# Kernel optimization log

Hardware: AMD Instinct MI355X
Metric: run time of the kernel (lower is better)

Reference implementation:

```python
import jax, jax.numpy as jnp
from jax import lax
import numpy as np

BITS = 16
KSHAPE = (3, 5, 5)
STRIDE = (1, 1, 1)
PAD = (0, 0, 0)
IMG = (2048, 2048)


def setup_inputs() -> dict:
    key = jax.random.key(0)
    k1, k2 = jax.random.split(key)
    x = jax.random.randint(k1, IMG, 0, 2 ** BITS, dtype=jnp.int32)
    weight = jax.random.uniform(k2, KSHAPE, dtype=jnp.float32)
    bias = jnp.zeros((1,), dtype=jnp.float32)
    return {"x": x, "weight": weight, "bias": bias}


def reference(x, weight, bias):
    pad_d, pad_h, pad_w = PAD
    # spatial zero-padding of the integer image
    xp = jnp.pad(x, ((pad_h, pad_h), (pad_w, pad_w)))
    # bit-plane volume: V[z] = bit z of each pixel. (x << pad_d >> s) % 2
    # equals bit (s - pad_d) of x, and is 0 for s < pad_d, i.e. depth
    # zero-padding by pad_d on both sides of the BITS bit-planes.
    z = jnp.arange(BITS, dtype=jnp.int32)
    V = ((xp[None, :, :] >> z[:, None, None]) & 1).astype(jnp.float32)
    V = jnp.pad(V, ((pad_d, pad_d), (0, 0), (0, 0)))  # [D, Hp, Wp]
    # 3D cross-correlation (lax conv does not flip the kernel)
    Y = lax.conv_general_dilated(
        V[None, None],               # [1,1,D,Hp,Wp]
        weight[None, None],          # [1,1,d,h,w]
        window_strides=STRIDE,
        padding="VALID",
        dimension_numbers=("NCDHW", "OIDHW", "NCDHW"),
    )[0, 0]                          # [D_out, H_out, W_out]
    return Y + bias
```

## Files before the change

kernel.cpp:

```cpp
#include <hip/hip_runtime.h>

#define IMG_W 2048
#define IMG_H 2048
#define OUT_W 2044
#define OUT_H 2044
#define OUT_HW (2044 * 2044)

#define TI 16
#define TJ 64
#define LR (TI + 4)
#define LC (TJ + 4)
#define LSTR 69

typedef int v4i __attribute__((ext_vector_type(4)));

__global__ void quant_frag(const float* __restrict__ w, v4i* __restrict__ wfrag) {
    const int l = threadIdx.x;
    const int m = l & 15, g = l >> 4;
    #pragma unroll
    for (int t = 0; t < 7; ++t) {
        const int p = 4 * t + g;
        unsigned lo[4] = {0, 0, 0, 0}, hi[4] = {0, 0, 0, 0};
        if (p < 25 && m < 14) {
            const int kh = p / 5, kw = p % 5;
            #pragma unroll
            for (int kd = 0; kd < 3; ++kd) {
                const int e = m + kd;
                const unsigned w8 = (unsigned)(int)rintf(w[(kd * 5 + kh) * 5 + kw] * 255.0f);
                lo[e >> 2] |= (w8 & 15u) << (8 * (e & 3));
                hi[e >> 2] |= (w8 >> 4)  << (8 * (e & 3));
            }
        }
        v4i vlo, vhi;
        vlo.x = (int)lo[0]; vlo.y = (int)lo[1]; vlo.z = (int)lo[2]; vlo.w = (int)lo[3];
        vhi.x = (int)hi[0]; vhi.y = (int)hi[1]; vhi.z = (int)hi[2]; vhi.w = (int)hi[3];
        wfrag[t * 64 + l]       = vlo;
        wfrag[448 + t * 64 + l] = vhi;
    }
}

__global__ __launch_bounds__(256, 3) void conv_mfma(
        const int* __restrict__ x, const v4i* __restrict__ wfrag,
        const float* __restrict__ bias, float* __restrict__ out) {
    __shared__ v4i vt[LR * LSTR];
    const int tid  = threadIdx.x;
    const int lane = tid & 63;
    const int wv   = tid >> 6;
    const int m16  = lane & 15;
    const int g4   = lane >> 4;
    const int I0 = blockIdx.y * TI;
    const int J0 = blockIdx.x * TJ;

    v4i alo[7], ahi[7];
    #pragma unroll
    for (int t = 0; t < 7; ++t) {
        alo[t] = wfrag[t * 64 + lane];
        ahi[t] = wfrag[448 + t * 64 + lane];
    }
    const float b0 = bias[0];

    #pragma unroll
    for (int rr = 0; rr < 5; ++rr) {
        const int r  = wv + rr * 4;
        const int gr = min(I0 + r, IMG_H - 1);
        const long rowoff = (long)gr * IMG_W;
        #pragma unroll
        for (int cc = 0; cc < 2; ++cc) {
            const int col = lane + cc * 64;
            if (col < LC) {
                const int gc = min(J0 + col, IMG_W - 1);
                const unsigned v = (unsigned)x[rowoff + gc];
                v4i e;
                e.x = (int)(__umul24( v         & 0xFu, 0x00204081u) & 0x01010101u);
                e.y = (int)(__umul24((v >> 4)   & 0xFu, 0x00204081u) & 0x01010101u);
                e.z = (int)(__umul24((v >> 8)   & 0xFu, 0x00204081u) & 0x01010101u);
                e.w = (int)(__umul24((v >> 12)  & 0xFu, 0x00204081u) & 0x01010101u);
                vt[r * LSTR + col] = e;
            }
        }
    }
    __syncthreads();

    int koff[7];
    #pragma unroll
    for (int t = 0; t < 7; ++t) {
        const int p  = 4 * t + g4;
        const int kh = (p < 25) ? (p / 5) : 0;
        const int kw = (p < 25) ? (p - kh * 5) : 0;
        koff[t] = kh * LSTR + kw;
    }

    const float scale = 1.0f / 255.0f;

    #pragma unroll 1
    for (int ig = 0; ig < 4; ++ig) {
        const int il = wv * 4 + ig;
        const int i  = I0 + il;
        #pragma unroll 1
        for (int jg = 0; jg < 4; ++jg) {
            const int jb    = jg * 16 + m16;
            const int gbase = il * LSTR + jb;
            v4i bf[7];
            #pragma unroll
            for (int t = 0; t < 7; ++t) bf[t] = vt[gbase + koff[t]];

            v4i al0 = {0,0,0,0}, al1 = {0,0,0,0}, ah0 = {0,0,0,0}, ah1 = {0,0,0,0};
            #pragma unroll
            for (int t = 0; t < 6; t += 2) {
                al0 = __builtin_amdgcn_mfma_i32_16x16x64_i8(alo[t],     bf[t],     al0, 0, 0, 0);
                ah0 = __builtin_amdgcn_mfma_i32_16x16x64_i8(ahi[t],     bf[t],     ah0, 0, 0, 0);
                al1 = __builtin_amdgcn_mfma_i32_16x16x64_i8(alo[t + 1], bf[t + 1], al1, 0, 0, 0);
                ah1 = __builtin_amdgcn_mfma_i32_16x16x64_i8(ahi[t + 1], bf[t + 1], ah1, 0, 0, 0);
            }
            al0 = __builtin_amdgcn_mfma_i32_16x16x64_i8(alo[6], bf[6], al0, 0, 0, 0);
            ah0 = __builtin_amdgcn_mfma_i32_16x16x64_i8(ahi[6], bf[6], ah0, 0, 0, 0);

            const int j = J0 + jb;
            if (i < OUT_H && j < OUT_W) {
                #pragma unroll
                for (int r = 0; r < 4; ++r) {
                    const int d = g4 * 4 + r;
                    if (d < 14) {
                        const int acc = (ah0[r] + ah1[r]) * 16 + (al0[r] + al1[r]);
                        out[(size_t)d * OUT_HW + (size_t)i * OUT_W + j] =
                            fmaf((float)acc, scale, b0);
                    }
                }
            }
        }
    }
}

extern "C" void kernel_launch(void* const* d_in, const int* in_sizes, int n_in,
                              void* d_out, int out_size, void* d_ws, size_t ws_size,
                              hipStream_t stream) {
    const int* x      = (const int*)d_in[0];
    const float* w    = (const float*)d_in[1];
    const float* bias = (const float*)d_in[2];
    float* out        = (float*)d_out;
    v4i* wfrag        = (v4i*)d_ws;

    quant_frag<<<1, 64, 0, stream>>>(w, wfrag);
    conv_mfma<<<dim3((OUT_W + TJ - 1) / TJ, (OUT_H + TI - 1) / TI), 256, 0, stream>>>(
        x, wfrag, bias, out);
}
```

Before: 301.5 us.

## Stage conv outputs through LDS transpose for fully coalesced row stores

Each wave now writes its MFMA results for a row into a padded per-wave LDS buffer, then reads them back transposed. Each lane can then store one output column across the 14 depth planes, so every store instruction covers 64 contiguous floats instead of four scattered 16-float segments. This targets global write efficiency on the very large output tensor. It adds LDS traffic and LDS footprint, lowers the launch-bounds occupancy hint from 3 to 2, and fully unrolls the jg loop. The 16-byte vector writes at a row stride of 17 floats may be misaligned for ds_write_b128.

```diff
diff --git a/kernel.cpp b/kernel.cpp
--- a/kernel.cpp
+++ b/kernel.cpp
@@ -11,8 +11,10 @@
 #define LR (TI + 4)
 #define LC (TJ + 4)
 #define LSTR 69
+#define TRP 17
 
 typedef int v4i __attribute__((ext_vector_type(4)));
+typedef float v4f __attribute__((ext_vector_type(4)));
 
 __global__ void quant_frag(const float* __restrict__ w, v4i* __restrict__ wfrag) {
     const int l = threadIdx.x;
@@ -39,10 +41,11 @@
     }
 }
 
-__global__ __launch_bounds__(256, 3) void conv_mfma(
+__global__ __launch_bounds__(256, 2) void conv_mfma(
         const int* __restrict__ x, const v4i* __restrict__ wfrag,
         const float* __restrict__ bias, float* __restrict__ out) {
     __shared__ v4i vt[LR * LSTR];
+    __shared__ float trp[4 * 64 * TRP];
     const int tid  = threadIdx.x;
     const int lane = tid & 63;
     const int wv   = tid >> 6;
@@ -91,18 +94,18 @@
     }
 
     const float scale = 1.0f / 255.0f;
+    float* twr = trp + wv * (64 * TRP);
 
     #pragma unroll 1
-    for (int ig = 0; ig < 4; ++ig) {
-        const int il = wv * 4 + ig;
-        const int i  = I0 + il;
-        #pragma unroll 1
+    for (int il_ = 0; il_ < 4; ++il_) {
+        const int il = wv * 4 + il_;
+
+        #pragma unroll
         for (int jg = 0; jg < 4; ++jg) {
-            const int jb    = jg * 16 + m16;
-            const int gbase = il * LSTR + jb;
+            const int rec = il * LSTR + jg * 16 + m16;
             v4i bf[7];
             #pragma unroll
-            for (int t = 0; t < 7; ++t) bf[t] = vt[gbase + koff[t]];
+            for (int t = 0; t < 7; ++t) bf[t] = vt[rec + koff[t]];
 
             v4i al0 = {0,0,0,0}, al1 = {0,0,0,0}, ah0 = {0,0,0,0}, ah1 = {0,0,0,0};
             #pragma unroll
@@ -115,17 +118,24 @@
             al0 = __builtin_amdgcn_mfma_i32_16x16x64_i8(alo[6], bf[6], al0, 0, 0, 0);
             ah0 = __builtin_amdgcn_mfma_i32_16x16x64_i8(ahi[6], bf[6], ah0, 0, 0, 0);
 
-            const int j = J0 + jb;
-            if (i < OUT_H && j < OUT_W) {
-                #pragma unroll
-                for (int r = 0; r < 4; ++r) {
-                    const int d = g4 * 4 + r;
-                    if (d < 14) {
-                        const int acc = (ah0[r] + ah1[r]) * 16 + (al0[r] + al1[r]);
-                        out[(size_t)d * OUT_HW + (size_t)i * OUT_W + j] =
-                            fmaf((float)acc, scale, b0);
-                    }
-                }
+            v4f o;
+            #pragma unroll
+            for (int r = 0; r < 4; ++r) {
+                const int acc = (ah0[r] + ah1[r]) * 16 + (al0[r] + al1[r]);
+                o[r] = fmaf((float)acc, scale, b0);
+            }
+            *(v4f*)(twr + (jg * 16 + m16) * TRP + g4 * 4) = o;
+        }
+
+        const int i = I0 + il;
+        if (i < OUT_H) {
+            const int j = J0 + lane;
+            const float* tb = twr + lane * TRP;
+            float* ob = out + (size_t)i * OUT_W + j;
+            const bool jok = j < OUT_W;
+            #pragma unroll
+            for (int d = 0; d < 14; ++d) {
+                if (jok) ob[(size_t)d * OUT_HW] = tb[d];
             }
         }
     }
```

Measured after the change: 293.3 us. 2.7% less time.
